# Kernel optimization log

Measured on AMD Instinct MI355X. Metric: run time of the kernel, lower is better.

The kernel has to match this reference:

```python
import jax, jax.numpy as jnp
import numpy as np

TOP_K = 8

def setup_inputs() -> dict:
    key = jax.random.key(0)
    k1, k2 = jax.random.split(key)
    hidden_states = jax.random.normal(k1, (4, 4096, 2048), dtype=jnp.float32)
    weight = jax.random.normal(k2, (64, 2048), dtype=jnp.float32) * 0.02
    return {"hidden_states": hidden_states, "weight": weight}

def reference(hidden_states, weight):
    b, s, h = hidden_states.shape
    x = hidden_states.reshape(-1, h).astype(jnp.float32)   # [T, H]
    logits = jnp.einsum('th,eh->te', x, weight.astype(jnp.float32))  # [T, E]
    scores = jax.nn.softmax(logits, axis=-1)               # greedy router: softmax then top-k
    topk_weights, topk_idx = jax.lax.top_k(scores, TOP_K)  # [T, k]
    # renormalize top-k probabilities (norm_topk_prob)
    topk_weights = topk_weights / jnp.sum(topk_weights, axis=-1, keepdims=True)
    return topk_weights, topk_idx
```

## Files before the change

### kernel.cpp

```cpp
#include <hip/hip_runtime.h>
#include <math.h>


#define H_DIM 2048
#define N_EXP 64
#define TOPK 8
#define TOK 32

typedef __attribute__((ext_vector_type(8))) short bf16x8;
typedef __attribute__((ext_vector_type(4))) float f32x4;

union FragU { uint4 q; unsigned u[4]; bf16x8 s; };

__device__ inline unsigned cvt_pk_bf16(float lo, float hi) {
  unsigned d;
  asm("v_cvt_pk_bf16_f32 %0, %1, %2" : "=v"(d) : "v"(lo), "v"(hi));
  return d;
}

__device__ inline void split3(const float* e, unsigned* dh, unsigned* dm,
                              unsigned* dl) {
#pragma unroll
  for (int p = 0; p < 4; ++p) {
    const float f0 = e[2 * p], f1 = e[2 * p + 1];
    const unsigned h = cvt_pk_bf16(f0, f1);
    const float r0 = f0 - __uint_as_float(h << 16);
    const float r1 = f1 - __uint_as_float(h & 0xffff0000u);
    const unsigned m = cvt_pk_bf16(r0, r1);
    const float s0 = r0 - __uint_as_float(m << 16);
    const float s1 = r1 - __uint_as_float(m & 0xffff0000u);
    dl[p] = cvt_pk_bf16(s0, s1);
    dh[p] = h;
    dm[p] = m;
  }
}

__global__ __launch_bounds__(256) void w_split_kernel(
    const float* __restrict__ w, uint4* __restrict__ ws) {
  const int id = blockIdx.x * 256 + threadIdx.x;
  const int l = id & 63;
  const int nt = (id >> 6) & 3;
  const int ksg = id >> 8;
  const int n = nt * 16 + (l & 15);
  const int kb = ksg * 32 + ((l >> 4) << 3);
  const float* wr = w + (size_t)n * H_DIM + kb;
  const float4 a = *(const float4*)(wr);
  const float4 b = *(const float4*)(wr + 4);
  const float e[8] = {a.x, a.y, a.z, a.w, b.x, b.y, b.z, b.w};
  unsigned dh[4], dm[4], dl[4];
  split3(e, dh, dm, dl);
  const int base = (ksg * 12 + nt * 3) * 64 + l;
  ws[base] = make_uint4(dh[0], dh[1], dh[2], dh[3]);
  ws[base + 64] = make_uint4(dm[0], dm[1], dm[2], dm[3]);
  ws[base + 128] = make_uint4(dl[0], dl[1], dl[2], dl[3]);
}

__global__ __launch_bounds__(512, 2) void moe_gate_kernel(
    const float* __restrict__ x, const uint4* __restrict__ wf_g,
    float* __restrict__ out, int n_tokens) {
  __shared__ float part[8 * 2048];
  __shared__ float logits[N_EXP * TOK];

  const int tid = threadIdx.x;
  const int l = tid & 63;
  const int w = tid >> 6;
  const int kq = __builtin_amdgcn_readfirstlane(w);
  const int t0 = blockIdx.x * TOK;

  const float* xp0 =
      x + (size_t)(t0 + (l & 15)) * H_DIM + kq * 256 + ((l >> 4) << 3);
  const float* xp1 = xp0 + (size_t)16 * H_DIM;

  f32x4 acc[2][4];
#pragma unroll
  for (int t = 0; t < 2; ++t)
#pragma unroll
    for (int nt = 0; nt < 4; ++nt) acc[t][nt] = (f32x4){0.f, 0.f, 0.f, 0.f};

  float4 xa[2][2], xb[2][2], xc[2][2];
  xa[0][0] = *(const float4*)(xp0);
  xa[0][1] = *(const float4*)(xp0 + 4);
  xa[1][0] = *(const float4*)(xp1);
  xa[1][1] = *(const float4*)(xp1 + 4);
  xb[0][0] = *(const float4*)(xp0 + 32);
  xb[0][1] = *(const float4*)(xp0 + 36);
  xb[1][0] = *(const float4*)(xp1 + 32);
  xb[1][1] = *(const float4*)(xp1 + 36);

  const uint4* wbase = wf_g + (size_t)(kq * 8) * 768 + l;

#pragma unroll 1
  for (int s = 0; s < 8; ++s) {
    uint4 wf[12];
    const uint4* wb = wbase + (size_t)s * 768;
#pragma unroll
    for (int i = 0; i < 12; ++i) wf[i] = wb[i * 64];

    if (s + 2 < 8) {
      const float* p0 = xp0 + (s + 2) * 32;
      const float* p1 = xp1 + (s + 2) * 32;
      xc[0][0] = *(const float4*)(p0);
      xc[0][1] = *(const float4*)(p0 + 4);
      xc[1][0] = *(const float4*)(p1);
      xc[1][1] = *(const float4*)(p1 + 4);
    }

    bf16x8 ah[2], am[2], al[2];
#pragma unroll
    for (int t = 0; t < 2; ++t) {
      const float4 v0 = xa[t][0], v1 = xa[t][1];
      const float e[8] = {v0.x, v0.y, v0.z, v0.w, v1.x, v1.y, v1.z, v1.w};
      FragU uh, um, ul;
      split3(e, uh.u, um.u, ul.u);
      ah[t] = uh.s;
      am[t] = um.s;
      al[t] = ul.s;
    }

#pragma unroll
    for (int nt = 0; nt < 4; ++nt) {
      FragU bh, bm, bl;
      bh.q = wf[nt * 3 + 0];
      bm.q = wf[nt * 3 + 1];
      bl.q = wf[nt * 3 + 2];
#pragma unroll
      for (int t = 0; t < 2; ++t) {
        f32x4 c = acc[t][nt];
        c = __builtin_amdgcn_mfma_f32_16x16x32_bf16(ah[t], bh.s, c, 0, 0, 0);
        c = __builtin_amdgcn_mfma_f32_16x16x32_bf16(am[t], bh.s, c, 0, 0, 0);
        c = __builtin_amdgcn_mfma_f32_16x16x32_bf16(ah[t], bm.s, c, 0, 0, 0);
        c = __builtin_amdgcn_mfma_f32_16x16x32_bf16(al[t], bh.s, c, 0, 0, 0);
        c = __builtin_amdgcn_mfma_f32_16x16x32_bf16(ah[t], bl.s, c, 0, 0, 0);
        c = __builtin_amdgcn_mfma_f32_16x16x32_bf16(am[t], bm.s, c, 0, 0, 0);
        acc[t][nt] = c;
      }
    }

#pragma unroll
    for (int t = 0; t < 2; ++t)
#pragma unroll
      for (int h = 0; h < 2; ++h) {
        xa[t][h] = xb[t][h];
        xb[t][h] = xc[t][h];
      }
  }

#pragma unroll
  for (int t = 0; t < 2; ++t)
#pragma unroll
    for (int nt = 0; nt < 4; ++nt)
      *(float4*)&part[w * 2048 + (t * 4 + nt) * 256 + l * 4] =
          make_float4(acc[t][nt][0], acc[t][nt][1], acc[t][nt][2],
                      acc[t][nt][3]);
  __syncthreads();

  for (int z = tid; z < N_EXP * TOK; z += 512) {
    const int e = z >> 5, t32 = z & 31;
    const int tz = t32 >> 4, r16 = t32 & 15;
    const int q = r16 >> 2, rz = r16 & 3;
    const int idx = (tz * 4 + (e >> 4)) * 256 + (q * 16 + (e & 15)) * 4 + rz;
    float v = ((part[0 * 2048 + idx] + part[1 * 2048 + idx]) +
               (part[2 * 2048 + idx] + part[3 * 2048 + idx])) +
              ((part[4 * 2048 + idx] + part[5 * 2048 + idx]) +
               (part[6 * 2048 + idx] + part[7 * 2048 + idx]));
    logits[z] = v;
  }
  __syncthreads();

  if (tid >= TOK) return;

  float lg[N_EXP];
#pragma unroll
  for (int e = 0; e < N_EXP; ++e) lg[e] = logits[e * TOK + tid];

  float bw[TOPK];
  int bi[TOPK];
#pragma unroll
  for (int k = 0; k < TOPK; ++k) {
    float m = lg[0];
    int mi = 0;
#pragma unroll
    for (int e = 1; e < N_EXP; ++e) {
      if (lg[e] > m) {
        m = lg[e];
        mi = e;
      }
    }
    bw[k] = m;
    bi[k] = mi;
#pragma unroll
    for (int e = 0; e < N_EXP; ++e)
      if (e == mi) lg[e] = -INFINITY;
  }

  const float mx = bw[0];
  float ew[TOPK];
  float s = 0.f;
#pragma unroll
  for (int k = 0; k < TOPK; ++k) {
    ew[k] = expf(bw[k] - mx);
    s += ew[k];
  }
  const float inv = 1.f / s;

  float4 w0, w1, i0, i1;
  w0.x = ew[0] * inv; w0.y = ew[1] * inv; w0.z = ew[2] * inv; w0.w = ew[3] * inv;
  w1.x = ew[4] * inv; w1.y = ew[5] * inv; w1.z = ew[6] * inv; w1.w = ew[7] * inv;
  i0.x = (float)bi[0]; i0.y = (float)bi[1]; i0.z = (float)bi[2]; i0.w = (float)bi[3];
  i1.x = (float)bi[4]; i1.y = (float)bi[5]; i1.z = (float)bi[6]; i1.w = (float)bi[7];

  const int t = t0 + tid;
  float4* ow = reinterpret_cast<float4*>(out + (size_t)t * TOPK);
  ow[0] = w0;
  ow[1] = w1;
  float4* oi =
      reinterpret_cast<float4*>(out + (size_t)n_tokens * TOPK + (size_t)t * TOPK);
  oi[0] = i0;
  oi[1] = i1;
}

extern "C" void kernel_launch(void* const* d_in, const int* in_sizes, int n_in,
                              void* d_out, int out_size, void* d_ws,
                              size_t ws_size, hipStream_t stream) {
  const float* x = (const float*)d_in[0];
  const float* w = (const float*)d_in[1];
  float* out = (float*)d_out;
  const int n_tokens = in_sizes[0] / H_DIM;
  w_split_kernel<<<64, 256, 0, stream>>>(w, (uint4*)d_ws);
  const int n_blocks = n_tokens / TOK;
  moe_gate_kernel<<<n_blocks, 512, 0, stream>>>(x, (const uint4*)d_ws, out,
                                                n_tokens);
}
```

Before: 218.1 us.

## Split token halves across waves and double-buffer weight fragments in registers

Each wave now handles 16 tokens over a 512-wide K slice instead of 32 tokens over 256, so the cross-wave LDS reduction sums 4 partials instead of 8 and the shared-memory partial buffer is halved. Weight fragments are split into two 6-register buffers that are refilled one step ahead, interleaved with the MFMA halves, to hide global-load latency. The cost is that each wave reloads the full weight slice for its K range, so every weight fragment is fetched by two waves, and per-wave weight traffic goes up.

```diff
diff --git a/kernel.cpp b/kernel.cpp
--- a/kernel.cpp
+++ b/kernel.cpp
@@ -6,6 +6,7 @@
 #define N_EXP 64
 #define TOPK 8
 #define TOK 32
+#define NSTEP 16
 
 typedef __attribute__((ext_vector_type(8))) short bf16x8;
 typedef __attribute__((ext_vector_type(4))) float f32x4;
@@ -55,114 +56,103 @@
   ws[base + 128] = make_uint4(dl[0], dl[1], dl[2], dl[3]);
 }
 
+__device__ __forceinline__ void load_b6(uint4 (&dst)[6], const uint4* wb,
+                                        int off) {
+#pragma unroll
+  for (int i = 0; i < 6; ++i) dst[i] = wb[(off + i) * 64];
+}
+
+__device__ __forceinline__ void load_x2(float4 (&dst)[2], const float* p) {
+  dst[0] = *(const float4*)(p);
+  dst[1] = *(const float4*)(p + 4);
+}
+
+__device__ __forceinline__ void mfma_half(const bf16x8& ah, const bf16x8& am,
+                                          const bf16x8& al,
+                                          const uint4 (&bfr)[6],
+                                          f32x4 (&acc)[4], int nt0) {
+#pragma unroll
+  for (int j = 0; j < 2; ++j) {
+    FragU bh, bm, bl;
+    bh.q = bfr[j * 3 + 0];
+    bm.q = bfr[j * 3 + 1];
+    bl.q = bfr[j * 3 + 2];
+    f32x4 c = acc[nt0 + j];
+    c = __builtin_amdgcn_mfma_f32_16x16x32_bf16(ah, bh.s, c, 0, 0, 0);
+    c = __builtin_amdgcn_mfma_f32_16x16x32_bf16(am, bh.s, c, 0, 0, 0);
+    c = __builtin_amdgcn_mfma_f32_16x16x32_bf16(ah, bm.s, c, 0, 0, 0);
+    c = __builtin_amdgcn_mfma_f32_16x16x32_bf16(al, bh.s, c, 0, 0, 0);
+    c = __builtin_amdgcn_mfma_f32_16x16x32_bf16(ah, bl.s, c, 0, 0, 0);
+    c = __builtin_amdgcn_mfma_f32_16x16x32_bf16(am, bm.s, c, 0, 0, 0);
+    acc[nt0 + j] = c;
+  }
+}
+
 __global__ __launch_bounds__(512, 2) void moe_gate_kernel(
     const float* __restrict__ x, const uint4* __restrict__ wf_g,
     float* __restrict__ out, int n_tokens) {
-  __shared__ float part[8 * 2048];
+  __shared__ float part[8 * 1024];
   __shared__ float logits[N_EXP * TOK];
 
   const int tid = threadIdx.x;
   const int l = tid & 63;
   const int w = tid >> 6;
-  const int kq = __builtin_amdgcn_readfirstlane(w);
+  const int tp = w & 1;
+  const int kq = w >> 1;
   const int t0 = blockIdx.x * TOK;
 
-  const float* xp0 =
-      x + (size_t)(t0 + (l & 15)) * H_DIM + kq * 256 + ((l >> 4) << 3);
-  const float* xp1 = xp0 + (size_t)16 * H_DIM;
-
-  f32x4 acc[2][4];
-#pragma unroll
-  for (int t = 0; t < 2; ++t)
-#pragma unroll
-    for (int nt = 0; nt < 4; ++nt) acc[t][nt] = (f32x4){0.f, 0.f, 0.f, 0.f};
-
-  float4 xa[2][2], xb[2][2], xc[2][2];
-  xa[0][0] = *(const float4*)(xp0);
-  xa[0][1] = *(const float4*)(xp0 + 4);
-  xa[1][0] = *(const float4*)(xp1);
-  xa[1][1] = *(const float4*)(xp1 + 4);
-  xb[0][0] = *(const float4*)(xp0 + 32);
-  xb[0][1] = *(const float4*)(xp0 + 36);
-  xb[1][0] = *(const float4*)(xp1 + 32);
-  xb[1][1] = *(const float4*)(xp1 + 36);
-
-  const uint4* wbase = wf_g + (size_t)(kq * 8) * 768 + l;
+  const float* xp =
+      x + (size_t)(t0 + tp * 16 + (l & 15)) * H_DIM + kq * 512 + ((l >> 4) << 3);
+  const uint4* wbase = wf_g + (size_t)(kq * 16) * 768 + l;
+
+  f32x4 acc[4];
+#pragma unroll
+  for (int nt = 0; nt < 4; ++nt) acc[nt] = (f32x4){0.f, 0.f, 0.f, 0.f};
+
+  uint4 bA[6], bB[6];
+  float4 xA[2], xB[2], xC[2];
+
+  load_b6(bA, wbase, 0);
+  load_b6(bB, wbase, 6);
+  load_x2(xA, xp);
+  load_x2(xB, xp + 32);
 
 #pragma unroll 1
-  for (int s = 0; s < 8; ++s) {
-    uint4 wf[12];
-    const uint4* wb = wbase + (size_t)s * 768;
-#pragma unroll
-    for (int i = 0; i < 12; ++i) wf[i] = wb[i * 64];
-
-    if (s + 2 < 8) {
-      const float* p0 = xp0 + (s + 2) * 32;
-      const float* p1 = xp1 + (s + 2) * 32;
-      xc[0][0] = *(const float4*)(p0);
-      xc[0][1] = *(const float4*)(p0 + 4);
-      xc[1][0] = *(const float4*)(p1);
-      xc[1][1] = *(const float4*)(p1 + 4);
-    }
-
-    bf16x8 ah[2], am[2], al[2];
-#pragma unroll
-    for (int t = 0; t < 2; ++t) {
-      const float4 v0 = xa[t][0], v1 = xa[t][1];
+  for (int s = 0; s < NSTEP; ++s) {
+    bf16x8 ah, am, al;
+    {
+      const float4 v0 = xA[0], v1 = xA[1];
       const float e[8] = {v0.x, v0.y, v0.z, v0.w, v1.x, v1.y, v1.z, v1.w};
       FragU uh, um, ul;
       split3(e, uh.u, um.u, ul.u);
-      ah[t] = uh.s;
-      am[t] = um.s;
-      al[t] = ul.s;
+      ah = uh.s;
+      am = um.s;
+      al = ul.s;
     }
-
-#pragma unroll
-    for (int nt = 0; nt < 4; ++nt) {
-      FragU bh, bm, bl;
-      bh.q = wf[nt * 3 + 0];
-      bm.q = wf[nt * 3 + 1];
-      bl.q = wf[nt * 3 + 2];
-#pragma unroll
-      for (int t = 0; t < 2; ++t) {
-        f32x4 c = acc[t][nt];
-        c = __builtin_amdgcn_mfma_f32_16x16x32_bf16(ah[t], bh.s, c, 0, 0, 0);
-        c = __builtin_amdgcn_mfma_f32_16x16x32_bf16(am[t], bh.s, c, 0, 0, 0);
-        c = __builtin_amdgcn_mfma_f32_16x16x32_bf16(ah[t], bm.s, c, 0, 0, 0);
-        c = __builtin_amdgcn_mfma_f32_16x16x32_bf16(al[t], bh.s, c, 0, 0, 0);
-        c = __builtin_amdgcn_mfma_f32_16x16x32_bf16(ah[t], bl.s, c, 0, 0, 0);
-        c = __builtin_amdgcn_mfma_f32_16x16x32_bf16(am[t], bm.s, c, 0, 0, 0);
-        acc[t][nt] = c;
-      }
-    }
-
-#pragma unroll
-    for (int t = 0; t < 2; ++t)
-#pragma unroll
-      for (int h = 0; h < 2; ++h) {
-        xa[t][h] = xb[t][h];
-        xb[t][h] = xc[t][h];
-      }
-  }
-
-#pragma unroll
-  for (int t = 0; t < 2; ++t)
-#pragma unroll
-    for (int nt = 0; nt < 4; ++nt)
-      *(float4*)&part[w * 2048 + (t * 4 + nt) * 256 + l * 4] =
-          make_float4(acc[t][nt][0], acc[t][nt][1], acc[t][nt][2],
-                      acc[t][nt][3]);
+    mfma_half(ah, am, al, bA, acc, 0);
+    if (s + 1 < NSTEP) load_b6(bA, wbase + (size_t)(s + 1) * 768, 0);
+    if (s + 2 < NSTEP) load_x2(xC, xp + (s + 2) * 32);
+    mfma_half(ah, am, al, bB, acc, 2);
+    if (s + 1 < NSTEP) load_b6(bB, wbase + (size_t)(s + 1) * 768, 6);
+    xA[0] = xB[0]; xA[1] = xB[1];
+    xB[0] = xC[0]; xB[1] = xC[1];
+  }
+
+#pragma unroll
+  for (int nt = 0; nt < 4; ++nt)
+    *(float4*)&part[w * 1024 + nt * 256 + l * 4] =
+        make_float4(acc[nt][0], acc[nt][1], acc[nt][2], acc[nt][3]);
   __syncthreads();
 
   for (int z = tid; z < N_EXP * TOK; z += 512) {
     const int e = z >> 5, t32 = z & 31;
-    const int tz = t32 >> 4, r16 = t32 & 15;
+    const int tpz = t32 >> 4, r16 = t32 & 15;
     const int q = r16 >> 2, rz = r16 & 3;
-    const int idx = (tz * 4 + (e >> 4)) * 256 + (q * 16 + (e & 15)) * 4 + rz;
-    float v = ((part[0 * 2048 + idx] + part[1 * 2048 + idx]) +
-               (part[2 * 2048 + idx] + part[3 * 2048 + idx])) +
-              ((part[4 * 2048 + idx] + part[5 * 2048 + idx]) +
-               (part[6 * 2048 + idx] + part[7 * 2048 + idx]));
+    const int idx = (e >> 4) * 256 + (q * 16 + (e & 15)) * 4 + rz;
+    float v = ((part[(0 * 2 + tpz) * 1024 + idx] +
+                part[(1 * 2 + tpz) * 1024 + idx]) +
+               (part[(2 * 2 + tpz) * 1024 + idx] +
+                part[(3 * 2 + tpz) * 1024 + idx]));
     logits[z] = v;
   }
   __syncthreads();
```

Measured after the change: 226.8 us. 4.0% more time.
